# Optimization experiments

Hardware: AMD Instinct MI355X
Metric: run time of the kernel (lower is better)

Reference implementation:

```python
import jax, jax.numpy as jnp
import numpy as np

EPS = 1e-6
TEMP_GEO = 0.07
W_LOCAL = 0.5
W_SHARP = 0.5


def _l2norm(x):
    return x / jnp.clip(jnp.linalg.norm(x, axis=-1, keepdims=True), 1e-12)


def setup_inputs() -> dict:
    key = jax.random.key(0)
    ks = jax.random.split(key, 6)
    B, L, S, C = 8, 1024, 1024, 128
    N, P = 8, 256
    q_geo = _l2norm(jax.random.normal(ks[0], (B, L, C), jnp.float32))
    geo_pos = _l2norm(jax.random.normal(ks[1], (B, S, C), jnp.float32))
    label = jax.random.randint(ks[2], (B, L, S), 0, 2, jnp.int32)
    q_cl = jax.random.normal(ks[3], (N, P, C), jnp.float32)
    cl_pos = jax.random.normal(ks[4], (N, P, C), jnp.float32)
    idx = jax.random.randint(ks[5], (N,), 0, P, jnp.int32)
    return {"q_geo": q_geo, "q_cl": q_cl, "geo_pos": geo_pos,
            "cl_pos": cl_pos, "label": label, "idx": idx}


def _masked_mean(v, m):
    # per-sample mean over the [L,S] plane of entries where m is True
    m = m.astype(v.dtype)
    return jnp.sum(v * m, axis=(1, 2)) / jnp.maximum(jnp.sum(m, axis=(1, 2)), 1.0)


def _loftr_loss(conf, label):
    # standard LoFTR coarse CE loss (LoFTRLoss source absent from repo snippet)
    conf = jnp.clip(conf, EPS, 1.0 - EPS)
    pos = label == 1
    neg = label == 0
    pos_loss = _masked_mean(-jnp.log(conf), pos)          # [B]
    neg_loss = _masked_mean(-jnp.log(1.0 - conf), neg)    # [B]
    loss = pos_loss + neg_loss
    return jnp.mean(loss), jnp.mean(pos_loss), jnp.mean(neg_loss)


def _geometric_loss(q, k, label):
    sim = jnp.einsum('blc,bsc->bls', q, k) / TEMP_GEO        # [B,L,S]
    conf = jax.nn.softmax(sim, axis=1) * jax.nn.softmax(sim, axis=2)
    return _loftr_loss(conf, label)


def _sharpness_loss(q, k, label):
    sim = (1.0 + jnp.einsum('blc,bsc->bls', q, k)) / 2.0     # [B,L,S]
    # column stats (over L, dim=0 per sample) -> sharpness1 [B,S]
    s1 = (jnp.max(sim, axis=1) - jnp.mean(sim, axis=1)) / jnp.std(sim, axis=1, ddof=1)
    sharp1 = jax.nn.softmax(s1, axis=-1)
    # row stats (over S, dim=1 per sample) -> sharpness2 [B,L]
    s2 = (jnp.max(sim, axis=2) - jnp.mean(sim, axis=2)) / jnp.std(sim, axis=2, ddof=1)
    sharp2 = jax.nn.softmax(s2, axis=-1)
    simc = jnp.clip(sim, EPS, 1.0 - EPS)
    nll = -jnp.log(simc)
    pos = (label == 1).astype(simc.dtype)
    neg = (label == 0)
    loss1 = jnp.sum(nll * sharp1[:, None, :] * pos, axis=(1, 2))   # [B]
    loss2 = jnp.sum(nll * sharp2[:, :, None] * pos, axis=(1, 2))   # [B]
    loss3 = _masked_mean(-jnp.log(1.0 - simc), neg)                # [B]
    losses = (loss1 + loss2) / 2.0 + loss3
    return sharp1, jnp.mean(losses)


def _contrast_loss(q, all_k):
    # intended math of GeCoContrast: full cosine matrix, diag positives, tail negatives
    N = q.shape[0]
    sim = (1.0 + _l2norm(q) @ _l2norm(all_k).T) / 2.0   # [N, M]
    sim = jnp.clip(sim, EPS, 1.0 - EPS)
    l_pos = jnp.diagonal(sim[:, :N])                    # [N]
    l_neg = sim[:, N:]                                  # [N, M-N]
    return (jnp.mean(-jnp.log(l_pos)) + jnp.mean(-jnp.log(1.0 - l_neg))) / 2.0


def _forward(q_geo, q_cl, geo_pos, cl_pos, label, idx):
    loss_geo, geo_pos_loss, geo_neg_loss = _geometric_loss(q_geo, geo_pos, label)
    sharpness, loss_sharp = _sharpness_loss(q_geo, geo_pos, label)
    loss_geo = ((1.0 - W_SHARP) * loss_geo + W_SHARP * loss_sharp) * W_LOCAL

    N, P, C = q_cl.shape
    ar = jnp.arange(N)
    q_sel = q_cl[ar, idx]                               # [N,C]
    sel = cl_pos[ar, idx]                               # [N,C] positives moved to slot 0
    first = cl_pos[:, 0, :]
    swapped = cl_pos.at[ar, idx].set(first).at[:, 0, :].set(sel)
    cl_pos_save = sel
    all_k = jnp.concatenate([swapped[:, 0, :],
                             swapped[:, 1:, :].reshape(N * (P - 1), C)], axis=0)
    loss_cl = _contrast_loss(q_sel, all_k) * (1.0 - W_LOCAL)

    total = loss_geo + loss_cl
    return (sharpness, cl_pos_save, total, geo_pos_loss, geo_neg_loss, loss_sharp, loss_cl)


def reference(q_geo, q_cl, geo_pos, cl_pos, label, idx):
    return _forward(q_geo, q_cl, geo_pos, cl_pos, label, idx)
```

## Files before the change

### kernel.cpp

```cpp
#include <hip/hip_runtime.h>
#include <math.h>

#define BB 8
#define LL 1024
#define SS 1024
#define CC 128
#define NN 8
#define PP 256

static constexpr float EPS       = 1e-6f;
static constexpr float ONE_M_EPS = 1.0f - 1e-6f;
static constexpr float INV_T     = 1.0f / 0.07f;
static constexpr float NLL_MAX   = 13.815511f;
static constexpr float NLL_MIN   = 1.0000005e-6f;

static constexpr size_t DOTSZ      = (size_t)BB * LL * SS;
static constexpr size_t OFF_LSER   = DOTSZ;
static constexpr size_t OFF_S2RAW  = DOTSZ + 8192;
static constexpr size_t OFF_LSEC   = DOTSZ + 16384;
static constexpr size_t OFF_S1RAW  = DOTSZ + 24576;
static constexpr size_t OFF_SHARP2 = DOTSZ + 32768;
static constexpr size_t OFF_RP     = DOTSZ + 40960;
static constexpr size_t OFF_CP     = OFF_RP + 262144;
static constexpr size_t OFF_ACC    = OFF_RP + 524288;
static constexpr size_t OFF_ACCCL  = OFF_ACC + 48;
static constexpr size_t OFF_QN     = OFF_ACC + 64;

static constexpr int OUT_CLSAVE = 8192;
static constexpr int OUT_SCAL   = 9216;

typedef __bf16 bf16x8 __attribute__((ext_vector_type(8)));
typedef float  floatx4 __attribute__((ext_vector_type(4)));

#define LSTR 40

__device__ __forceinline__ void split_bf16(float x, short& hi, short& lo) {
    unsigned u = __builtin_bit_cast(unsigned, x);
    unsigned r = (u + 0x7FFFu + ((u >> 16) & 1u)) & 0xFFFF0000u;
    hi = (short)(r >> 16);
    float res = x - __builtin_bit_cast(float, r);
    unsigned u2 = __builtin_bit_cast(unsigned, res);
    lo = (short)((u2 + 0x7FFFu + ((u2 >> 16) & 1u)) >> 16);
}

__global__ __launch_bounds__(512) void prep(const float* __restrict__ q_cl,
                                            const float* __restrict__ cl_pos,
                                            const int* __restrict__ idx,
                                            float* __restrict__ out, float* __restrict__ ws) {
    int tid = threadIdx.x;
    if (tid < 50) ws[OFF_ACC + tid] = 0.0f;
    int n = tid >> 6, lane = tid & 63;
    int in = idx[n];
    const float* q = q_cl + ((size_t)(n * PP + in)) * CC;
    float2 qv = *(const float2*)(q + 2 * lane);
    float ss = qv.x * qv.x + qv.y * qv.y;
    for (int o = 32; o; o >>= 1) ss += __shfl_xor(ss, o);
    float inv = 1.0f / fmaxf(sqrtf(ss), 1e-12f);
    *(float2*)(ws + OFF_QN + n * 128 + 2 * lane) = make_float2(qv.x * inv, qv.y * inv);
    const float* cp = cl_pos + ((size_t)(n * PP + in)) * CC;
    float2 cv = *(const float2*)(cp + 2 * lane);
    *(float2*)(out + OUT_CLSAVE + n * 128 + 2 * lane) = cv;
}

__global__ __launch_bounds__(256) void gemm_dot(const float* __restrict__ A,
                                                const float* __restrict__ Bm,
                                                float* __restrict__ dot,
                                                float* __restrict__ ws) {
    int b  = blockIdx.z;
    int lt = blockIdx.y;
    int st = blockIdx.x;
    int l0 = lt * 128;
    int s0 = st * 128;
    __shared__ short Ah[128 * LSTR];
    __shared__ short Al[128 * LSTR];
    __shared__ short Bh[128 * LSTR];
    __shared__ short Bl[128 * LSTR];
    __shared__ float rowLDS[2][128][4];
    __shared__ float colLDS[2][128][4];

    int tid  = threadIdx.x;
    int lane = tid & 63;
    int w    = tid >> 6;
    int wr   = (w >> 1) * 64;
    int wc   = (w & 1) * 64;
    int fl   = lane & 15;
    int quad = lane >> 4;

    const float* Ab = A  + ((size_t)b * LL + l0) * CC;
    const float* Bb = Bm + ((size_t)b * SS + s0) * CC;

    floatx4 acc[4][4];
#pragma unroll
    for (int i = 0; i < 4; i++)
#pragma unroll
        for (int j = 0; j < 4; j++) acc[i][j] = (floatx4){0.f, 0.f, 0.f, 0.f};

    for (int c0 = 0; c0 < 128; c0 += 32) {
        if (c0) __syncthreads();
#pragma unroll
        for (int rep = 0; rep < 4; rep++) {
            int slot = tid + rep * 256;
            int row  = slot >> 3;
            int c4   = (slot & 7) * 4;
            float4 a4 = *(const float4*)(Ab + (size_t)row * CC + c0 + c4);
            float4 b4 = *(const float4*)(Bb + (size_t)row * CC + c0 + c4);
            short4 ah, al, bh, bl;
            split_bf16(a4.x, ah.x, al.x); split_bf16(a4.y, ah.y, al.y);
            split_bf16(a4.z, ah.z, al.z); split_bf16(a4.w, ah.w, al.w);
            split_bf16(b4.x, bh.x, bl.x); split_bf16(b4.y, bh.y, bl.y);
            split_bf16(b4.z, bh.z, bl.z); split_bf16(b4.w, bh.w, bl.w);
            int off = row * LSTR + c4;
            *(short4*)(Ah + off) = ah; *(short4*)(Al + off) = al;
            *(short4*)(Bh + off) = bh; *(short4*)(Bl + off) = bl;
        }
        __syncthreads();

        bf16x8 afh[4], afl[4];
#pragma unroll
        for (int mt = 0; mt < 4; mt++) {
            int off = (wr + mt * 16 + fl) * LSTR + quad * 8;
            afh[mt] = *reinterpret_cast<const bf16x8*>(Ah + off);
            afl[mt] = *reinterpret_cast<const bf16x8*>(Al + off);
        }
#pragma unroll
        for (int nt = 0; nt < 4; nt++) {
            int off = (wc + nt * 16 + fl) * LSTR + quad * 8;
            bf16x8 bfh = *reinterpret_cast<const bf16x8*>(Bh + off);
            bf16x8 bfl = *reinterpret_cast<const bf16x8*>(Bl + off);
#pragma unroll
            for (int mt = 0; mt < 4; mt++) {
                acc[mt][nt] = __builtin_amdgcn_mfma_f32_16x16x32_bf16(afh[mt], bfh, acc[mt][nt], 0, 0, 0);
                acc[mt][nt] = __builtin_amdgcn_mfma_f32_16x16x32_bf16(afh[mt], bfl, acc[mt][nt], 0, 0, 0);
                acc[mt][nt] = __builtin_amdgcn_mfma_f32_16x16x32_bf16(afl[mt], bfh, acc[mt][nt], 0, 0, 0);
            }
        }
    }

    float* D = dot + ((size_t)b * LL + l0) * SS + s0;
#pragma unroll
    for (int mt = 0; mt < 4; mt++)
#pragma unroll
        for (int nt = 0; nt < 4; nt++) {
            int col = wc + nt * 16 + fl;
#pragma unroll
            for (int r = 0; r < 4; r++) {
                int row = wr + mt * 16 + quad * 4 + r;
                D[(size_t)row * SS + col] = acc[mt][nt][r];
            }
        }

    float ces[4], cmx[4], csm[4], csq[4];
#pragma unroll
    for (int nt = 0; nt < 4; nt++) { ces[nt] = 0.f; cmx[nt] = -1e30f; csm[nt] = 0.f; csq[nt] = 0.f; }
#pragma unroll
    for (int mt = 0; mt < 4; mt++) {
#pragma unroll
        for (int r = 0; r < 4; r++) {
            float es = 0.f, mx = -1e30f, sm = 0.f, sq = 0.f;
#pragma unroll
            for (int nt = 0; nt < 4; nt++) {
                float d  = acc[mt][nt][r];
                float e  = __expf(d * INV_T);
                float s2 = fmaf(0.5f, d, 0.5f);
                es += e; mx = fmaxf(mx, s2); sm += s2; sq += s2 * s2;
                ces[nt] += e; cmx[nt] = fmaxf(cmx[nt], s2); csm[nt] += s2; csq[nt] += s2 * s2;
            }
            for (int o = 1; o < 16; o <<= 1) {
                es += __shfl_xor(es, o);
                mx = fmaxf(mx, __shfl_xor(mx, o));
                sm += __shfl_xor(sm, o);
                sq += __shfl_xor(sq, o);
            }
            if (fl == 0) {
                int rib = wr + mt * 16 + quad * 4 + r;
                rowLDS[w & 1][rib][0] = es; rowLDS[w & 1][rib][1] = mx;
                rowLDS[w & 1][rib][2] = sm; rowLDS[w & 1][rib][3] = sq;
            }
        }
    }
#pragma unroll
    for (int nt = 0; nt < 4; nt++) {
        float es = ces[nt], mx = cmx[nt], sm = csm[nt], sq = csq[nt];
        for (int o = 16; o < 64; o <<= 1) {
            es += __shfl_xor(es, o);
            mx = fmaxf(mx, __shfl_xor(mx, o));
            sm += __shfl_xor(sm, o);
            sq += __shfl_xor(sq, o);
        }
        if (quad == 0) {
            int cib = wc + nt * 16 + fl;
            colLDS[w >> 1][cib][0] = es; colLDS[w >> 1][cib][1] = mx;
            colLDS[w >> 1][cib][2] = sm; colLDS[w >> 1][cib][3] = sq;
        }
    }
    __syncthreads();
    if (tid < 128) {
        int rr = tid;
        float es = rowLDS[0][rr][0] + rowLDS[1][rr][0];
        float mx = fmaxf(rowLDS[0][rr][1], rowLDS[1][rr][1]);
        float sm = rowLDS[0][rr][2] + rowLDS[1][rr][2];
        float sq = rowLDS[0][rr][3] + rowLDS[1][rr][3];
        float4 v = make_float4(es, mx, sm, sq);
        *(float4*)(ws + OFF_RP + (((size_t)(b * 8 + st)) * 1024 + l0 + rr) * 4) = v;
    } else {
        int cc = tid - 128;
        float es = colLDS[0][cc][0] + colLDS[1][cc][0];
        float mx = fmaxf(colLDS[0][cc][1], colLDS[1][cc][1]);
        float sm = colLDS[0][cc][2] + colLDS[1][cc][2];
        float sq = colLDS[0][cc][3] + colLDS[1][cc][3];
        float4 v = make_float4(es, mx, sm, sq);
        *(float4*)(ws + OFF_CP + (((size_t)(b * 8 + lt)) * 1024 + s0 + cc) * 4) = v;
    }
}

__global__ __launch_bounds__(256) void rc_combine(float* __restrict__ ws) {
    int g = (blockIdx.x & 31) * 256 + threadIdx.x;
    bool docol = blockIdx.x >= 32;
    int b = g >> 10, i = g & 1023;
    const float* part = ws + (docol ? OFF_CP : OFF_RP);
    float es = 0.f, mx = -1e30f, sm = 0.f, sq = 0.f;
#pragma unroll
    for (int t = 0; t < 8; t++) {
        float4 v = *(const float4*)(part + (((size_t)(b * 8 + t)) * 1024 + i) * 4);
        es += v.x; mx = fmaxf(mx, v.y); sm += v.z; sq += v.w;
    }
    float mean = sm * (1.0f / 1024.0f);
    float var  = (sq - sm * sm * (1.0f / 1024.0f)) * (1.0f / 1023.0f);
    float zs   = (mx - mean) / sqrtf(fmaxf(var, 1e-30f));
    if (!docol) {
        ws[OFF_LSER + g]  = __logf(es);
        ws[OFF_S2RAW + g] = zs;
    } else {
        ws[OFF_LSEC + g]  = __logf(es);
        ws[OFF_S1RAW + g] = zs;
    }
}

__global__ __launch_bounds__(256) void softmax16(float* __restrict__ ws, float* __restrict__ out) {
    int q = blockIdx.x;
    int b = q & 7;
    const float* src = ws + ((q < 8) ? OFF_S1RAW : OFF_S2RAW) + (size_t)b * 1024;
    float* dst = (q < 8) ? (out + (size_t)b * 1024) : (ws + OFF_SHARP2 + (size_t)b * 1024);
    float4 v = ((const float4*)src)[threadIdx.x];
    int lane = threadIdx.x & 63, wid = threadIdx.x >> 6;
    __shared__ float sb[4];
    __shared__ float red;
    float mx = fmaxf(fmaxf(v.x, v.y), fmaxf(v.z, v.w));
    for (int o = 32; o; o >>= 1) mx = fmaxf(mx, __shfl_xor(mx, o));
    if (!lane) sb[wid] = mx;
    __syncthreads();
    if (threadIdx.x == 0) red = fmaxf(fmaxf(sb[0], sb[1]), fmaxf(sb[2], sb[3]));
    __syncthreads();
    mx = red;
    float e0 = __expf(v.x - mx), e1 = __expf(v.y - mx), e2 = __expf(v.z - mx), e3 = __expf(v.w - mx);
    float sm = e0 + e1 + e2 + e3;
    for (int o = 32; o; o >>= 1) sm += __shfl_xor(sm, o);
    __syncthreads();
    if (!lane) sb[wid] = sm;
    __syncthreads();
    if (threadIdx.x == 0) red = sb[0] + sb[1] + sb[2] + sb[3];
    __syncthreads();
    float inv = 1.0f / red;
    ((float4*)dst)[threadIdx.x] = make_float4(e0 * inv, e1 * inv, e2 * inv, e3 * inv);
}

__device__ __forceinline__ void proc_elem(float d, int lab, float lcj, float sh1j,
                                          float lr, float s2v,
                                          float& posg, float& negg, float& l1, float& l2,
                                          float& negs, float& pcf) {
    float t = lr + lcj - d * (2.0f * INV_T);
    float isPos = (lab == 1) ? 1.0f : 0.0f;
    float isNeg = 1.0f - isPos;
    float tp   = fminf(fmaxf(t, NLL_MIN), NLL_MAX);
    float simc = fminf(fmaxf(fmaf(0.5f, d, 0.5f), EPS), ONE_M_EPS);
    float om   = fminf(fmaxf(fmaf(-0.5f, d, 0.5f), EPS), ONE_M_EPS);
    float nll2 = -__logf(simc);
    float cf   = fminf(fmaxf(__expf(-t), EPS), ONE_M_EPS);
    float nllg = -__logf(1.0f - cf);
    float nlls = -__logf(om);
    posg += isPos * tp;
    l1   += isPos * nll2 * sh1j;
    l2   += isPos * nll2 * s2v;
    pcf  += isPos;
    negg += isNeg * nllg;
    negs += isNeg * nlls;
}

__global__ __launch_bounds__(256) void main_loss(const float* __restrict__ dot,
                                                 const int* __restrict__ label,
                                                 const float* __restrict__ sharp1,
                                                 float* __restrict__ ws) {
    int b = blockIdx.y;
    int l0 = blockIdx.x * 4;
    int s = threadIdx.x * 4;
    float4 lc4 = *(const float4*)(ws + OFF_LSEC + (size_t)b * 1024 + s);
    float4 sh1 = *(const float4*)(sharp1 + (size_t)b * 1024 + s);
    const float* lser = ws + OFF_LSER + (size_t)b * 1024;
    const float* sh2  = ws + OFF_SHARP2 + (size_t)b * 1024;
    float posg = 0, negg = 0, l1 = 0, l2 = 0, negs = 0, pcf = 0;
#pragma unroll
    for (int r = 0; r < 4; r++) {
        int l = l0 + r;
        float lr  = lser[l];
        float s2v = sh2[l];
        size_t base = ((size_t)(b * 1024 + l)) * 1024 + s;
        float4 d4 = *(const float4*)(dot + base);
        int4  lb  = *(const int4*)(label + base);
        proc_elem(d4.x, lb.x, lc4.x, sh1.x, lr, s2v, posg, negg, l1, l2, negs, pcf);
        proc_elem(d4.y, lb.y, lc4.y, sh1.y, lr, s2v, posg, negg, l1, l2, negs, pcf);
        proc_elem(d4.z, lb.z, lc4.z, sh1.z, lr, s2v, posg, negg, l1, l2, negs, pcf);
        proc_elem(d4.w, lb.w, lc4.w, sh1.w, lr, s2v, posg, negg, l1, l2, negs, pcf);
    }
    float vals[6] = {posg, negg, l1, l2, negs, pcf};
    __shared__ float sb[6][4];
    int lane = threadIdx.x & 63, wid = threadIdx.x >> 6;
#pragma unroll
    for (int k = 0; k < 6; k++) {
        float v = vals[k];
        for (int o = 32; o; o >>= 1) v += __shfl_xor(v, o);
        if (!lane) sb[k][wid] = v;
    }
    __syncthreads();
    if (threadIdx.x < 6) {
        float r = sb[threadIdx.x][0] + sb[threadIdx.x][1] + sb[threadIdx.x][2] + sb[threadIdx.x][3];
        atomicAdd(ws + OFF_ACC + (size_t)b * 6 + threadIdx.x, r);
    }
}

__global__ __launch_bounds__(256) void contrast(const float* __restrict__ cl_pos,
                                                const int* __restrict__ idx,
                                                float* __restrict__ ws) {
    int j = blockIdx.x * 4 + (threadIdx.x >> 6);
    int lane = threadIdx.x & 63;
    int m, p;
    if (j < NN) {
        m = j; p = idx[j];
    } else {
        int jj = j - NN;
        m = jj / (PP - 1);
        p = 1 + (jj - m * (PP - 1));
        if (p == idx[m]) p = 0;
    }
    const float* k = cl_pos + ((size_t)(m * PP + p)) * CC;
    float2 kv = *(const float2*)(k + 2 * lane);
    float ksq = kv.x * kv.x + kv.y * kv.y;
    for (int o = 32; o; o >>= 1) ksq += __shfl_xor(ksq, o);
    float invkn = 1.0f / fmaxf(sqrtf(ksq), 1e-12f);
    float pos = 0.0f, neg = 0.0f;
    if (j < NN) {
        const float2 qv = *(const float2*)(ws + OFF_QN + j * 128 + 2 * lane);
        float dt = qv.x * kv.x + qv.y * kv.y;
        for (int o = 32; o; o >>= 1) dt += __shfl_xor(dt, o);
        float sim = fminf(fmaxf(fmaf(0.5f * invkn, dt, 0.5f), EPS), ONE_M_EPS);
        pos = -__logf(sim);
    } else {
#pragma unroll
        for (int n = 0; n < NN; n++) {
            const float2 qv = *(const float2*)(ws + OFF_QN + n * 128 + 2 * lane);
            float dt = qv.x * kv.x + qv.y * kv.y;
            for (int o = 32; o; o >>= 1) dt += __shfl_xor(dt, o);
            float om = fminf(fmaxf(fmaf(-0.5f * invkn, dt, 0.5f), EPS), ONE_M_EPS);
            neg -= __logf(om);
        }
    }
    __shared__ float sb[2][4];
    int w = threadIdx.x >> 6;
    if (!lane) { sb[0][w] = pos; sb[1][w] = neg; }
    __syncthreads();
    if (threadIdx.x == 0) {
        float ps = sb[0][0] + sb[0][1] + sb[0][2] + sb[0][3];
        float ng = sb[1][0] + sb[1][1] + sb[1][2] + sb[1][3];
        if (ps != 0.0f) atomicAdd(ws + OFF_ACCCL + 0, ps);
        if (ng != 0.0f) atomicAdd(ws + OFF_ACCCL + 1, ng);
    }
}

__global__ void finalize(float* __restrict__ out, const float* __restrict__ ws) {
    if (threadIdx.x != 0) return;
    float gp = 0, gn = 0, lsh = 0;
    for (int b = 0; b < 8; b++) {
        const float* a = ws + OFF_ACC + (size_t)b * 6;
        float pc = a[5];
        float nc = (float)((size_t)LL * SS) - pc;
        gp += a[0] / fmaxf(pc, 1.0f);
        gn += a[1] / fmaxf(nc, 1.0f);
        lsh += (a[2] + a[3]) * 0.5f + a[4] / fmaxf(nc, 1.0f);
    }
    gp *= 0.125f; gn *= 0.125f; lsh *= 0.125f;
    float lgeo = gp + gn;
    float lgw = (0.5f * lgeo + 0.5f * lsh) * 0.5f;
    float clp = ws[OFF_ACCCL + 0] / 8.0f;
    float cln = ws[OFF_ACCCL + 1] / (8.0f * 2040.0f);
    float lcl = (clp + cln) * 0.5f * 0.5f;
    out[OUT_SCAL + 0] = lgw + lcl;
    out[OUT_SCAL + 1] = gp;
    out[OUT_SCAL + 2] = gn;
    out[OUT_SCAL + 3] = lsh;
    out[OUT_SCAL + 4] = lcl;
}

extern "C" void kernel_launch(void* const* d_in, const int* in_sizes, int n_in,
                              void* d_out, int out_size, void* d_ws, size_t ws_size,
                              hipStream_t stream) {
    const float* q_geo   = (const float*)d_in[0];
    const float* q_cl    = (const float*)d_in[1];
    const float* geo_pos = (const float*)d_in[2];
    const float* cl_pos  = (const float*)d_in[3];
    const int*   label   = (const int*)d_in[4];
    const int*   idx     = (const int*)d_in[5];
    float* out = (float*)d_out;
    float* ws  = (float*)d_ws;
    float* dot = ws;

    prep<<<dim3(1), dim3(512), 0, stream>>>(q_cl, cl_pos, idx, out, ws);
    gemm_dot<<<dim3(8, 8, 8), dim3(256), 0, stream>>>(q_geo, geo_pos, dot, ws);
    rc_combine<<<dim3(64), dim3(256), 0, stream>>>(ws);
    softmax16<<<dim3(16), dim3(256), 0, stream>>>(ws, out);
    main_loss<<<dim3(256, 8), dim3(256), 0, stream>>>(dot, label, out, ws);
    contrast<<<dim3(512), dim3(256), 0, stream>>>(cl_pos, idx, ws);
    finalize<<<dim3(1), dim3(64), 0, stream>>>(out, ws);
}
```

Measured before the change: 167.5 us.

## Make each wave compute an independent 64x64 tile directly from global memory

The GEMM kernel drops the shared-memory staging and block-wide synchronisation. Each wave now loads its own A/B fragments straight from global memory, splits them into hi/lo bf16 in registers with perm-based packing, and computes a private 64x64 tile. The row and column partial statistics are written directly per wave, which doubles the partial count to 16 per row/column, so the workspace layout and the combine kernel are adjusted to match. This removes LDS traffic and barriers but gives up sharing of operands between waves, so there is more redundant global/L2 loading and split arithmetic per tile.

```diff
diff --git a/kernel.cpp b/kernel.cpp
--- a/kernel.cpp
+++ b/kernel.cpp
@@ -21,8 +21,8 @@
 static constexpr size_t OFF_S1RAW  = DOTSZ + 24576;
 static constexpr size_t OFF_SHARP2 = DOTSZ + 32768;
 static constexpr size_t OFF_RP     = DOTSZ + 40960;
-static constexpr size_t OFF_CP     = OFF_RP + 262144;
-static constexpr size_t OFF_ACC    = OFF_RP + 524288;
+static constexpr size_t OFF_CP     = OFF_RP + 524288;
+static constexpr size_t OFF_ACC    = OFF_CP + 524288;
 static constexpr size_t OFF_ACCCL  = OFF_ACC + 48;
 static constexpr size_t OFF_QN     = OFF_ACC + 64;
 
@@ -32,15 +32,32 @@
 typedef __bf16 bf16x8 __attribute__((ext_vector_type(8)));
 typedef float  floatx4 __attribute__((ext_vector_type(4)));
 
-#define LSTR 40
-
-__device__ __forceinline__ void split_bf16(float x, short& hi, short& lo) {
-    unsigned u = __builtin_bit_cast(unsigned, x);
-    unsigned r = (u + 0x7FFFu + ((u >> 16) & 1u)) & 0xFFFF0000u;
-    hi = (short)(r >> 16);
-    float res = x - __builtin_bit_cast(float, r);
-    unsigned u2 = __builtin_bit_cast(unsigned, res);
-    lo = (short)((u2 + 0x7FFFu + ((u2 >> 16) & 1u)) >> 16);
+__device__ __forceinline__ bf16x8 mkfrag(unsigned a, unsigned b, unsigned c, unsigned d) {
+    uint4 t = make_uint4(a, b, c, d);
+    return __builtin_bit_cast(bf16x8, t);
+}
+
+__device__ __forceinline__ void split_f4(float4 x,
+                                         unsigned& hp0, unsigned& hp1,
+                                         unsigned& lp0, unsigned& lp1) {
+    unsigned u0 = __builtin_bit_cast(unsigned, x.x);
+    unsigned u1 = __builtin_bit_cast(unsigned, x.y);
+    unsigned u2 = __builtin_bit_cast(unsigned, x.z);
+    unsigned u3 = __builtin_bit_cast(unsigned, x.w);
+    unsigned r0 = u0 + 0x7FFFu + ((u0 >> 16) & 1u);
+    unsigned r1 = u1 + 0x7FFFu + ((u1 >> 16) & 1u);
+    unsigned r2 = u2 + 0x7FFFu + ((u2 >> 16) & 1u);
+    unsigned r3 = u3 + 0x7FFFu + ((u3 >> 16) & 1u);
+    float s0 = x.x - __builtin_bit_cast(float, r0 & 0xFFFF0000u);
+    float s1 = x.y - __builtin_bit_cast(float, r1 & 0xFFFF0000u);
+    float s2 = x.z - __builtin_bit_cast(float, r2 & 0xFFFF0000u);
+    float s3 = x.w - __builtin_bit_cast(float, r3 & 0xFFFF0000u);
+    hp0 = __builtin_amdgcn_perm(r1, r0, 0x07060302u);
+    hp1 = __builtin_amdgcn_perm(r3, r2, 0x07060302u);
+    lp0 = __builtin_amdgcn_perm(__builtin_bit_cast(unsigned, s1),
+                                __builtin_bit_cast(unsigned, s0), 0x07060302u);
+    lp1 = __builtin_amdgcn_perm(__builtin_bit_cast(unsigned, s3),
+                                __builtin_bit_cast(unsigned, s2), 0x07060302u);
 }
 
 __global__ __launch_bounds__(512) void prep(const float* __restrict__ q_cl,
@@ -66,23 +83,14 @@
                                                 const float* __restrict__ Bm,
                                                 float* __restrict__ dot,
                                                 float* __restrict__ ws) {
-    int b  = blockIdx.z;
-    int lt = blockIdx.y;
-    int st = blockIdx.x;
-    int l0 = lt * 128;
-    int s0 = st * 128;
-    __shared__ short Ah[128 * LSTR];
-    __shared__ short Al[128 * LSTR];
-    __shared__ short Bh[128 * LSTR];
-    __shared__ short Bl[128 * LSTR];
-    __shared__ float rowLDS[2][128][4];
-    __shared__ float colLDS[2][128][4];
-
     int tid  = threadIdx.x;
     int lane = tid & 63;
     int w    = tid >> 6;
-    int wr   = (w >> 1) * 64;
-    int wc   = (w & 1) * 64;
+    int t    = blockIdx.x * 4 + w;
+    int b    = t >> 8;
+    int rem  = t & 255;
+    int lt   = rem >> 4, st = rem & 15;
+    int l0   = lt * 64, s0 = st * 64;
     int fl   = lane & 15;
     int quad = lane >> 4;
 
@@ -96,42 +104,40 @@
         for (int j = 0; j < 4; j++) acc[i][j] = (floatx4){0.f, 0.f, 0.f, 0.f};
 
     for (int c0 = 0; c0 < 128; c0 += 32) {
-        if (c0) __syncthreads();
-#pragma unroll
-        for (int rep = 0; rep < 4; rep++) {
-            int slot = tid + rep * 256;
-            int row  = slot >> 3;
-            int c4   = (slot & 7) * 4;
-            float4 a4 = *(const float4*)(Ab + (size_t)row * CC + c0 + c4);
-            float4 b4 = *(const float4*)(Bb + (size_t)row * CC + c0 + c4);
-            short4 ah, al, bh, bl;
-            split_bf16(a4.x, ah.x, al.x); split_bf16(a4.y, ah.y, al.y);
-            split_bf16(a4.z, ah.z, al.z); split_bf16(a4.w, ah.w, al.w);
-            split_bf16(b4.x, bh.x, bl.x); split_bf16(b4.y, bh.y, bl.y);
-            split_bf16(b4.z, bh.z, bl.z); split_bf16(b4.w, bh.w, bl.w);
-            int off = row * LSTR + c4;
-            *(short4*)(Ah + off) = ah; *(short4*)(Al + off) = al;
-            *(short4*)(Bh + off) = bh; *(short4*)(Bl + off) = bl;
-        }
-        __syncthreads();
-
-        bf16x8 afh[4], afl[4];
+        float4 ax[4][2], bx[4][2];
 #pragma unroll
         for (int mt = 0; mt < 4; mt++) {
-            int off = (wr + mt * 16 + fl) * LSTR + quad * 8;
-            afh[mt] = *reinterpret_cast<const bf16x8*>(Ah + off);
-            afl[mt] = *reinterpret_cast<const bf16x8*>(Al + off);
+            const float* p = Ab + (size_t)(mt * 16 + fl) * CC + c0 + quad * 8;
+            ax[mt][0] = *(const float4*)p;
+            ax[mt][1] = *(const float4*)(p + 4);
         }
 #pragma unroll
         for (int nt = 0; nt < 4; nt++) {
-            int off = (wc + nt * 16 + fl) * LSTR + quad * 8;
-            bf16x8 bfh = *reinterpret_cast<const bf16x8*>(Bh + off);
-            bf16x8 bfl = *reinterpret_cast<const bf16x8*>(Bl + off);
+            const float* p = Bb + (size_t)(nt * 16 + fl) * CC + c0 + quad * 8;
+            bx[nt][0] = *(const float4*)p;
+            bx[nt][1] = *(const float4*)(p + 4);
+        }
+        bf16x8 ah[4], al[4];
+#pragma unroll
+        for (int mt = 0; mt < 4; mt++) {
+            unsigned h0, h1, h2, h3, q0, q1, q2, q3;
+            split_f4(ax[mt][0], h0, h1, q0, q1);
+            split_f4(ax[mt][1], h2, h3, q2, q3);
+            ah[mt] = mkfrag(h0, h1, h2, h3);
+            al[mt] = mkfrag(q0, q1, q2, q3);
+        }
+#pragma unroll
+        for (int nt = 0; nt < 4; nt++) {
+            unsigned h0, h1, h2, h3, q0, q1, q2, q3;
+            split_f4(bx[nt][0], h0, h1, q0, q1);
+            split_f4(bx[nt][1], h2, h3, q2, q3);
+            bf16x8 bh = mkfrag(h0, h1, h2, h3);
+            bf16x8 bl = mkfrag(q0, q1, q2, q3);
 #pragma unroll
             for (int mt = 0; mt < 4; mt++) {
-                acc[mt][nt] = __builtin_amdgcn_mfma_f32_16x16x32_bf16(afh[mt], bfh, acc[mt][nt], 0, 0, 0);
-                acc[mt][nt] = __builtin_amdgcn_mfma_f32_16x16x32_bf16(afh[mt], bfl, acc[mt][nt], 0, 0, 0);
-                acc[mt][nt] = __builtin_amdgcn_mfma_f32_16x16x32_bf16(afl[mt], bfh, acc[mt][nt], 0, 0, 0);
+                acc[mt][nt] = __builtin_amdgcn_mfma_f32_16x16x32_bf16(ah[mt], bh, acc[mt][nt], 0, 0, 0);
+                acc[mt][nt] = __builtin_amdgcn_mfma_f32_16x16x32_bf16(ah[mt], bl, acc[mt][nt], 0, 0, 0);
+                acc[mt][nt] = __builtin_amdgcn_mfma_f32_16x16x32_bf16(al[mt], bh, acc[mt][nt], 0, 0, 0);
             }
         }
     }
@@ -141,10 +147,10 @@
     for (int mt = 0; mt < 4; mt++)
 #pragma unroll
         for (int nt = 0; nt < 4; nt++) {
-            int col = wc + nt * 16 + fl;
+            int col = nt * 16 + fl;
 #pragma unroll
             for (int r = 0; r < 4; r++) {
-                int row = wr + mt * 16 + quad * 4 + r;
+                int row = mt * 16 + quad * 4 + r;
                 D[(size_t)row * SS + col] = acc[mt][nt][r];
             }
         }
@@ -172,9 +178,9 @@
                 sq += __shfl_xor(sq, o);
             }
             if (fl == 0) {
-                int rib = wr + mt * 16 + quad * 4 + r;
-                rowLDS[w & 1][rib][0] = es; rowLDS[w & 1][rib][1] = mx;
-                rowLDS[w & 1][rib][2] = sm; rowLDS[w & 1][rib][3] = sq;
+                int row = l0 + mt * 16 + quad * 4 + r;
+                *(float4*)(ws + OFF_RP + (((size_t)(b * 16 + st)) * 1024 + row) * 4) =
+                    make_float4(es, mx, sm, sq);
             }
         }
     }
@@ -188,28 +194,10 @@
             sq += __shfl_xor(sq, o);
         }
         if (quad == 0) {
-            int cib = wc + nt * 16 + fl;
-            colLDS[w >> 1][cib][0] = es; colLDS[w >> 1][cib][1] = mx;
-            colLDS[w >> 1][cib][2] = sm; colLDS[w >> 1][cib][3] = sq;
-        }
-    }
-    __syncthreads();
-    if (tid < 128) {
-        int rr = tid;
-        float es = rowLDS[0][rr][0] + rowLDS[1][rr][0];
-        float mx = fmaxf(rowLDS[0][rr][1], rowLDS[1][rr][1]);
-        float sm = rowLDS[0][rr][2] + rowLDS[1][rr][2];
-        float sq = rowLDS[0][rr][3] + rowLDS[1][rr][3];
-        float4 v = make_float4(es, mx, sm, sq);
-        *(float4*)(ws + OFF_RP + (((size_t)(b * 8 + st)) * 1024 + l0 + rr) * 4) = v;
-    } else {
-        int cc = tid - 128;
-        float es = colLDS[0][cc][0] + colLDS[1][cc][0];
-        float mx = fmaxf(colLDS[0][cc][1], colLDS[1][cc][1]);
-        float sm = colLDS[0][cc][2] + colLDS[1][cc][2];
-        float sq = colLDS[0][cc][3] + colLDS[1][cc][3];
-        float4 v = make_float4(es, mx, sm, sq);
-        *(float4*)(ws + OFF_CP + (((size_t)(b * 8 + lt)) * 1024 + s0 + cc) * 4) = v;
+            int col = s0 + nt * 16 + fl;
+            *(float4*)(ws + OFF_CP + (((size_t)(b * 16 + lt)) * 1024 + col) * 4) =
+                make_float4(es, mx, sm, sq);
+        }
     }
 }
 
@@ -220,8 +208,8 @@
     const float* part = ws + (docol ? OFF_CP : OFF_RP);
     float es = 0.f, mx = -1e30f, sm = 0.f, sq = 0.f;
 #pragma unroll
-    for (int t = 0; t < 8; t++) {
-        float4 v = *(const float4*)(part + (((size_t)(b * 8 + t)) * 1024 + i) * 4);
+    for (int t = 0; t < 16; t++) {
+        float4 v = *(const float4*)(part + (((size_t)(b * 16 + t)) * 1024 + i) * 4);
         es += v.x; mx = fmaxf(mx, v.y); sm += v.z; sq += v.w;
     }
     float mean = sm * (1.0f / 1024.0f);
@@ -413,7 +401,7 @@
     float* dot = ws;
 
     prep<<<dim3(1), dim3(512), 0, stream>>>(q_cl, cl_pos, idx, out, ws);
-    gemm_dot<<<dim3(8, 8, 8), dim3(256), 0, stream>>>(q_geo, geo_pos, dot, ws);
+    gemm_dot<<<dim3(512), dim3(256), 0, stream>>>(q_geo, geo_pos, dot, ws);
     rc_combine<<<dim3(64), dim3(256), 0, stream>>>(ws);
     softmax16<<<dim3(16), dim3(256), 0, stream>>>(ws, out);
     main_loss<<<dim3(256, 8), dim3(256), 0, stream>>>(dot, label, out, ws);
```

After: 163.7 us. 1.02x faster.
